# Kernel optimization log

Hardware: AMD Instinct MI355X
Metric: run time of the kernel (lower is better)

The kernel has to match this reference:

```python
import jax, jax.numpy as jnp
import numpy as np

N, D, K = 65536, 512, 5


def setup_inputs() -> dict:
    key = jax.random.key(0)
    k0, k1, k2, k3, k4 = jax.random.split(key, 5)
    x = jax.random.normal(k0, (N, D), dtype=jnp.float32)
    is_protected = jax.random.randint(k1, (N,), 0, 2) > 0  # bool mask
    alpha_p = jax.random.uniform(k2, (D,), dtype=jnp.float32, minval=0.9, maxval=1.1)
    classif_w = jax.random.normal(k3, (K, 1), dtype=jnp.float32)
    centroids = jax.random.normal(k4, (K, D), dtype=jnp.float32)
    return {"x": x, "is_protected": is_protected, "alpha_p": alpha_p,
            "classif_w": classif_w, "centroids": centroids}


def reference(x, is_protected, alpha_p, classif_w, centroids):
    # NOTE: original torch forward applies alpha_p to both the protected and
    # non-protected rows (alpha_np is unused), so the mask split is a no-op
    # and we compute the mapping over all rows at once.
    # distances: sum_d alpha_d * (x_nd - c_kd)^2  -> (n, k)
    diff2 = (x[:, None, :] - centroids[None, :, :]) ** 2  # (n, k, d)
    dist = jnp.einsum("nkd,d->nk", diff2, alpha_p)
    mapping = jax.nn.softmax(dist, axis=-1)              # (n, k)
    reconstructed = mapping @ centroids                  # (n, d)
    pred = (mapping @ jax.nn.sigmoid(classif_w)).ravel() # (n,)
    return mapping, reconstructed, pred
```

## Files before the change

### kernel.cpp

```cpp
#include <hip/hip_runtime.h>
#include <math.h>

#define LFR_N 65536
#define LFR_D 512
#define LFR_K 5

__global__ __launch_bounds__(256) void lfr_kernel(
    const float* __restrict__ x,
    const float* __restrict__ alpha,
    const float* __restrict__ w,
    const float* __restrict__ cent,
    float* __restrict__ out_map,
    float* __restrict__ out_rec,
    float* __restrict__ out_pred)
{
    const int lane           = threadIdx.x & 63;
    const int wave_in_block  = threadIdx.x >> 6;
    const int waves_per_blk  = blockDim.x >> 6;
    const int wave_id        = blockIdx.x * waves_per_blk + wave_in_block;
    const int num_waves      = gridDim.x * waves_per_blk;

    const int d0 = lane * 8;

    float al[8];
    {
        float4 a0 = *(const float4*)(alpha + d0);
        float4 a1 = *(const float4*)(alpha + d0 + 4);
        al[0]=a0.x; al[1]=a0.y; al[2]=a0.z; al[3]=a0.w;
        al[4]=a1.x; al[5]=a1.y; al[6]=a1.z; al[7]=a1.w;
    }
    float c[LFR_K][8];
    #pragma unroll
    for (int k = 0; k < LFR_K; ++k) {
        float4 c0 = *(const float4*)(cent + k * LFR_D + d0);
        float4 c1 = *(const float4*)(cent + k * LFR_D + d0 + 4);
        c[k][0]=c0.x; c[k][1]=c0.y; c[k][2]=c0.z; c[k][3]=c0.w;
        c[k][4]=c1.x; c[k][5]=c1.y; c[k][6]=c1.z; c[k][7]=c1.w;
    }
    float sigw[LFR_K];
    #pragma unroll
    for (int k = 0; k < LFR_K; ++k)
        sigw[k] = 1.0f / (1.0f + __expf(-w[k]));

    for (int row = wave_id; row < LFR_N; row += num_waves) {
        const float* xr = x + (size_t)row * LFR_D + d0;
        float xv[8];
        {
            float4 x0 = *(const float4*)(xr);
            float4 x1 = *(const float4*)(xr + 4);
            xv[0]=x0.x; xv[1]=x0.y; xv[2]=x0.z; xv[3]=x0.w;
            xv[4]=x1.x; xv[5]=x1.y; xv[6]=x1.z; xv[7]=x1.w;
        }

        float dist[LFR_K];
        #pragma unroll
        for (int k = 0; k < LFR_K; ++k) {
            float acc = 0.0f;
            #pragma unroll
            for (int j = 0; j < 8; ++j) {
                float df = xv[j] - c[k][j];
                acc = fmaf(al[j] * df, df, acc);
            }
            dist[k] = acc;
        }

        #pragma unroll
        for (int off = 32; off > 0; off >>= 1) {
            #pragma unroll
            for (int k = 0; k < LFR_K; ++k)
                dist[k] += __shfl_xor(dist[k], off);
        }

        float mx = dist[0];
        #pragma unroll
        for (int k = 1; k < LFR_K; ++k) mx = fmaxf(mx, dist[k]);
        float e[LFR_K], s = 0.0f;
        #pragma unroll
        for (int k = 0; k < LFR_K; ++k) { e[k] = __expf(dist[k] - mx); s += e[k]; }
        float inv = 1.0f / s;
        float m[LFR_K];
        #pragma unroll
        for (int k = 0; k < LFR_K; ++k) m[k] = e[k] * inv;

        float r[8];
        #pragma unroll
        for (int j = 0; j < 8; ++j) {
            float acc = m[0] * c[0][j];
            #pragma unroll
            for (int k = 1; k < LFR_K; ++k) acc = fmaf(m[k], c[k][j], acc);
            r[j] = acc;
        }
        float* rr = out_rec + (size_t)row * LFR_D + d0;
        *(float4*)(rr)     = make_float4(r[0], r[1], r[2], r[3]);
        *(float4*)(rr + 4) = make_float4(r[4], r[5], r[6], r[7]);

        if (lane < LFR_K) out_map[(size_t)row * LFR_K + lane] = m[lane];
        if (lane == 0) {
            float p = 0.0f;
            #pragma unroll
            for (int k = 0; k < LFR_K; ++k) p = fmaf(m[k], sigw[k], p);
            out_pred[row] = p;
        }
    }
}

extern "C" void kernel_launch(void* const* d_in, const int* in_sizes, int n_in,
                              void* d_out, int out_size, void* d_ws, size_t ws_size,
                              hipStream_t stream) {
    const float* x     = (const float*)d_in[0];
    const float* alpha = (const float*)d_in[2];
    const float* w     = (const float*)d_in[3];
    const float* cent  = (const float*)d_in[4];

    float* out   = (float*)d_out;
    float* o_map = out;
    float* o_rec = out + (size_t)LFR_N * LFR_K;
    float* o_prd = out + (size_t)LFR_N * LFR_K + (size_t)LFR_N * LFR_D;

    dim3 grid(2048), block(256);
    lfr_kernel<<<grid, block, 0, stream>>>(x, alpha, w, cent, o_map, o_rec, o_prd);
}
```

Before: 246.5 us.

## Expand weighted distance into dot products and map one thread per row

A one-block prep kernel precomputes alpha-scaled centroids, per-centroid bias terms and the sigmoid weights in the workspace. The main kernel then gives each thread a whole row, expanding the weighted squared distance into a bias minus twice a dot product. The per-row alpha*x^2 term is dropped because softmax ignores a per-row constant. This removes the cross-lane shuffle reductions, but each thread now walks its own 2 KB row, so x loads and reconstruction stores are strided across lanes rather than coalesced, and it adds a second launch.

```diff
diff --git a/kernel.cpp b/kernel.cpp
--- a/kernel.cpp
+++ b/kernel.cpp
@@ -5,102 +5,99 @@
 #define LFR_D 512
 #define LFR_K 5
 
-__global__ __launch_bounds__(256) void lfr_kernel(
+#define WS_AC 0
+#define WS_BK 2560
+#define WS_SW 2568
+
+__global__ __launch_bounds__(512) void lfr_prep(
+    const float* __restrict__ alpha, const float* __restrict__ w,
+    const float* __restrict__ cent, float* __restrict__ ws)
+{
+    const int t = threadIdx.x;
+    for (int f = t; f < LFR_K * LFR_D; f += 512)
+        ws[WS_AC + f] = alpha[f & (LFR_D - 1)] * cent[f];
+    const int wv = t >> 6, l = t & 63;
+    if (wv < LFR_K) {
+        float s = 0.0f;
+        #pragma unroll
+        for (int j = 0; j < 8; ++j) {
+            int d = l * 8 + j;
+            float a = alpha[d], c = cent[wv * LFR_D + d];
+            s = fmaf(a * c, c, s);
+        }
+        #pragma unroll
+        for (int off = 32; off > 0; off >>= 1) s += __shfl_xor(s, off);
+        if (l == 0) ws[WS_BK + wv] = s;
+    }
+    if (t < LFR_K) ws[WS_SW + t] = 1.0f / (1.0f + __expf(-w[t]));
+}
+
+__global__ __launch_bounds__(128) void lfr_main(
     const float* __restrict__ x,
-    const float* __restrict__ alpha,
-    const float* __restrict__ w,
     const float* __restrict__ cent,
+    const float* __restrict__ ws,
     float* __restrict__ out_map,
     float* __restrict__ out_rec,
     float* __restrict__ out_pred)
 {
-    const int lane           = threadIdx.x & 63;
-    const int wave_in_block  = threadIdx.x >> 6;
-    const int waves_per_blk  = blockDim.x >> 6;
-    const int wave_id        = blockIdx.x * waves_per_blk + wave_in_block;
-    const int num_waves      = gridDim.x * waves_per_blk;
+    const int row = blockIdx.x * 128 + threadIdx.x;
+    const size_t base = (size_t)row * (LFR_D / 4);
 
-    const int d0 = lane * 8;
+    const float4* __restrict__ x4  = (const float4*)x;
+    const float4* __restrict__ ac4 = (const float4*)(ws + WS_AC);
+    const float4* __restrict__ c4  = (const float4*)cent;
 
-    float al[8];
-    {
-        float4 a0 = *(const float4*)(alpha + d0);
-        float4 a1 = *(const float4*)(alpha + d0 + 4);
-        al[0]=a0.x; al[1]=a0.y; al[2]=a0.z; al[3]=a0.w;
-        al[4]=a1.x; al[5]=a1.y; al[6]=a1.z; al[7]=a1.w;
+    float dot[LFR_K] = {0.f, 0.f, 0.f, 0.f, 0.f};
+    #pragma unroll 4
+    for (int q = 0; q < LFR_D / 4; ++q) {
+        float4 xv = x4[base + q];
+        #pragma unroll
+        for (int k = 0; k < LFR_K; ++k) {
+            float4 cq = ac4[k * (LFR_D / 4) + q];
+            dot[k] = fmaf(xv.x, cq.x, dot[k]);
+            dot[k] = fmaf(xv.y, cq.y, dot[k]);
+            dot[k] = fmaf(xv.z, cq.z, dot[k]);
+            dot[k] = fmaf(xv.w, cq.w, dot[k]);
+        }
     }
-    float c[LFR_K][8];
+
+    float m[LFR_K];
+    float mx = -3.402823466e38f;
     #pragma unroll
     for (int k = 0; k < LFR_K; ++k) {
-        float4 c0 = *(const float4*)(cent + k * LFR_D + d0);
-        float4 c1 = *(const float4*)(cent + k * LFR_D + d0 + 4);
-        c[k][0]=c0.x; c[k][1]=c0.y; c[k][2]=c0.z; c[k][3]=c0.w;
-        c[k][4]=c1.x; c[k][5]=c1.y; c[k][6]=c1.z; c[k][7]=c1.w;
+        m[k] = ws[WS_BK + k] - 2.0f * dot[k];
+        mx = fmaxf(mx, m[k]);
     }
-    float sigw[LFR_K];
+    float s = 0.0f;
     #pragma unroll
-    for (int k = 0; k < LFR_K; ++k)
-        sigw[k] = 1.0f / (1.0f + __expf(-w[k]));
+    for (int k = 0; k < LFR_K; ++k) { m[k] = __expf(m[k] - mx); s += m[k]; }
+    float inv = 1.0f / s;
+    #pragma unroll
+    for (int k = 0; k < LFR_K; ++k) m[k] *= inv;
 
-    for (int row = wave_id; row < LFR_N; row += num_waves) {
-        const float* xr = x + (size_t)row * LFR_D + d0;
-        float xv[8];
-        {
-            float4 x0 = *(const float4*)(xr);
-            float4 x1 = *(const float4*)(xr + 4);
-            xv[0]=x0.x; xv[1]=x0.y; xv[2]=x0.z; xv[3]=x0.w;
-            xv[4]=x1.x; xv[5]=x1.y; xv[6]=x1.z; xv[7]=x1.w;
-        }
+    {
+        float* mp = out_map + (size_t)row * LFR_K;
+        mp[0] = m[0]; mp[1] = m[1]; mp[2] = m[2]; mp[3] = m[3]; mp[4] = m[4];
+        float p = 0.0f;
+        #pragma unroll
+        for (int k = 0; k < LFR_K; ++k) p = fmaf(m[k], ws[WS_SW + k], p);
+        out_pred[row] = p;
+    }
 
-        float dist[LFR_K];
-        #pragma unroll
-        for (int k = 0; k < LFR_K; ++k) {
-            float acc = 0.0f;
-            #pragma unroll
-            for (int j = 0; j < 8; ++j) {
-                float df = xv[j] - c[k][j];
-                acc = fmaf(al[j] * df, df, acc);
-            }
-            dist[k] = acc;
-        }
-
-        #pragma unroll
-        for (int off = 32; off > 0; off >>= 1) {
-            #pragma unroll
-            for (int k = 0; k < LFR_K; ++k)
-                dist[k] += __shfl_xor(dist[k], off);
-        }
-
-        float mx = dist[0];
-        #pragma unroll
-        for (int k = 1; k < LFR_K; ++k) mx = fmaxf(mx, dist[k]);
-        float e[LFR_K], s = 0.0f;
-        #pragma unroll
-        for (int k = 0; k < LFR_K; ++k) { e[k] = __expf(dist[k] - mx); s += e[k]; }
-        float inv = 1.0f / s;
-        float m[LFR_K];
-        #pragma unroll
-        for (int k = 0; k < LFR_K; ++k) m[k] = e[k] * inv;
-
-        float r[8];
-        #pragma unroll
-        for (int j = 0; j < 8; ++j) {
-            float acc = m[0] * c[0][j];
-            #pragma unroll
-            for (int k = 1; k < LFR_K; ++k) acc = fmaf(m[k], c[k][j], acc);
-            r[j] = acc;
-        }
-        float* rr = out_rec + (size_t)row * LFR_D + d0;
-        *(float4*)(rr)     = make_float4(r[0], r[1], r[2], r[3]);
-        *(float4*)(rr + 4) = make_float4(r[4], r[5], r[6], r[7]);
-
-        if (lane < LFR_K) out_map[(size_t)row * LFR_K + lane] = m[lane];
-        if (lane == 0) {
-            float p = 0.0f;
-            #pragma unroll
-            for (int k = 0; k < LFR_K; ++k) p = fmaf(m[k], sigw[k], p);
-            out_pred[row] = p;
-        }
+    float4* __restrict__ r4 = (float4*)out_rec;
+    #pragma unroll 4
+    for (int q = 0; q < LFR_D / 4; ++q) {
+        float4 o;
+        float4 c0 = c4[0 * (LFR_D / 4) + q];
+        float4 c1 = c4[1 * (LFR_D / 4) + q];
+        float4 c2 = c4[2 * (LFR_D / 4) + q];
+        float4 c3 = c4[3 * (LFR_D / 4) + q];
+        float4 cq4 = c4[4 * (LFR_D / 4) + q];
+        o.x = fmaf(m[4], cq4.x, fmaf(m[3], c3.x, fmaf(m[2], c2.x, fmaf(m[1], c1.x, m[0] * c0.x))));
+        o.y = fmaf(m[4], cq4.y, fmaf(m[3], c3.y, fmaf(m[2], c2.y, fmaf(m[1], c1.y, m[0] * c0.y))));
+        o.z = fmaf(m[4], cq4.z, fmaf(m[3], c3.z, fmaf(m[2], c2.z, fmaf(m[1], c1.z, m[0] * c0.z))));
+        o.w = fmaf(m[4], cq4.w, fmaf(m[3], c3.w, fmaf(m[2], c2.w, fmaf(m[1], c1.w, m[0] * c0.w))));
+        r4[base + q] = o;
     }
 }
 
@@ -116,7 +113,9 @@
     float* o_map = out;
     float* o_rec = out + (size_t)LFR_N * LFR_K;
     float* o_prd = out + (size_t)LFR_N * LFR_K + (size_t)LFR_N * LFR_D;
+    float* ws    = (float*)d_ws;
 
-    dim3 grid(2048), block(256);
-    lfr_kernel<<<grid, block, 0, stream>>>(x, alpha, w, cent, o_map, o_rec, o_prd);
+    lfr_prep<<<dim3(1), dim3(512), 0, stream>>>(alpha, w, cent, ws);
+    lfr_main<<<dim3(LFR_N / 128), dim3(128), 0, stream>>>(
+        x, cent, ws, o_map, o_rec, o_prd);
 }
```

New measurement: 276.9 us. 12.3% more time.
